# Performance work log

Hardware: AMD Instinct MI355X
Metric: run time of the kernel (lower is better)

Reference implementation:

```python
import jax, jax.numpy as jnp
import numpy as np
from functools import partial

RES = 512          # image resolution (source uses 1024; scaled for CPU baseline)
BLOB_COUNT = 2048  # number of Gaussian blobs (source uses 4096)
CHUNK = 64         # blobs processed per scan step to bound intermediates


def setup_inputs() -> dict:
    key = jax.random.key(0)
    k_pos, k_scale, k_rot, k_col = jax.random.split(key, 4)
    pos = jax.random.uniform(k_pos, (BLOB_COUNT, 2))                      # blob centers in [0,1]^2
    scale = 0.005 + 0.05 * jax.random.uniform(k_scale, (BLOB_COUNT, 2))   # per-axis std dev
    rot = 2.0 * jnp.pi * jax.random.uniform(k_rot, (BLOB_COUNT, 1))       # rotation angle
    color = jax.random.uniform(k_col, (BLOB_COUNT, 3))                    # rgb intensity
    blobs = jnp.concatenate([pos, scale, rot, color], axis=-1).astype(jnp.float32)  # [N, 8]
    return {"blobs": blobs}


def _splat(blobs):
    H = W = RES
    # pixel centers in normalized [0,1] coords
    ys = (jnp.arange(H, dtype=jnp.float32) + 0.5) / H
    xs = (jnp.arange(W, dtype=jnp.float32) + 0.5) / W
    py, px = jnp.meshgrid(ys, xs, indexing="ij")  # [H, W]

    def body(img, chunk):  # chunk: [CHUNK, 8]
        pos = chunk[:, 0:2]
        sx = chunk[:, 2][:, None, None]
        sy = chunk[:, 3][:, None, None]
        rot = chunk[:, 4]
        color = chunk[:, 5:8]
        c = jnp.cos(rot)[:, None, None]
        s = jnp.sin(rot)[:, None, None]
        dx = px[None] - pos[:, 0][:, None, None]   # [C, H, W]
        dy = py[None] - pos[:, 1][:, None, None]
        xr = c * dx + s * dy                        # rotate into blob frame
        yr = -s * dx + c * dy
        g = jnp.exp(-0.5 * ((xr / sx) ** 2 + (yr / sy) ** 2))  # [C, H, W]
        img = img + jnp.einsum("chw,ck->hwk", g, color)
        return img, None

    img0 = jnp.zeros((H, W, 3), dtype=blobs.dtype)
    chunks = blobs.reshape(BLOB_COUNT // CHUNK, CHUNK, 8)
    img, _ = jax.lax.scan(jax.checkpoint(body), img0, chunks)
    return img


@jax.jit
def reference(blobs):
    return _splat(blobs)
```

## Files before the change

kernel.cpp:

```cpp
#include <hip/hip_runtime.h>
#include <math.h>

#define RES     512
#define NBLOB   2048
#define TILE_W  32
#define TILE_H  32
#define ROWS_T  8
#define TX_N    (RES / TILE_W)
#define TY_N    (RES / TILE_H)
#define PRE_STRIDE 16
#define CHUNK_B 256
#define NCHUNK  (NBLOB / CHUNK_B)
#define CULL_R  4.4055f

__device__ __forceinline__ float fast_exp2(float x) {
#if __has_builtin(__builtin_amdgcn_exp2f)
    return __builtin_amdgcn_exp2f(x);
#else
    return exp2f(x);
#endif
}

__global__ __launch_bounds__(256) void pre_kernel(const float* __restrict__ blobs,
                                                  float* __restrict__ pre) {
    int i = blockIdx.x * blockDim.x + threadIdx.x;
    if (i >= NBLOB) return;
    const float* bp = blobs + i * 8;
    float posx = bp[0], posy = bp[1];
    float sx = bp[2], sy = bp[3];
    float rot = bp[4];
    float c = cosf(rot), s = sinf(rot);
    const float K = 0.84932184f;
    float isx = K / sx, isy = K / sy;
    float* o = pre + i * PRE_STRIDE;
    o[0] = posx;
    o[1] = posy;
    o[2] = c * isx;
    o[3] = s * isx;
    o[4] = -s * isy;
    o[5] = c * isy;
    o[6] = bp[5];
    o[7] = bp[6];
    o[8] = bp[7];
    o[9] = 0.f; o[10] = 0.f; o[11] = 0.f;

    float hx = CULL_R * sqrtf(c * c * sx * sx + s * s * sy * sy);
    float hy = CULL_R * sqrtf(s * s * sx * sx + c * c * sy * sy);
    int tx0 = max(0,        (int)floorf(((posx - hx) * RES - 0.5f) * (1.0f / TILE_W)));
    int tx1 = min(TX_N - 1, (int)floorf(((posx + hx) * RES - 0.5f) * (1.0f / TILE_W)));
    int ty0 = max(0,        (int)floorf(((posy - hy) * RES - 0.5f) * (1.0f / TILE_H)));
    int ty1 = min(TY_N - 1, (int)floorf(((posy + hy) * RES - 0.5f) * (1.0f / TILE_H)));
    int* ob = (int*)(o + 12);
    ob[0] = tx0; ob[1] = tx1; ob[2] = ty0; ob[3] = ty1;
}

__global__ __launch_bounds__(256) void splat_kernel(const float* __restrict__ pre,
                                                    float* __restrict__ out) {
    __shared__ int sh_cnt[NCHUNK];
    __shared__ float4 sh_p0[CHUNK_B];
    __shared__ float4 sh_p1[CHUNK_B];
    __shared__ float  sh_p2[CHUNK_B];

    const int tid = threadIdx.x;
    const int lane = tid & 63;
    const int tx = blockIdx.x;
    const int ty = blockIdx.y;

    if (tid < NCHUNK) sh_cnt[tid] = 0;

    const int x  = tx * TILE_W + (tid & 31);
    const int y0 = ty * TILE_H + (tid >> 5);
    const float fx  = (x + 0.5f) * (1.0f / RES);
    const float fy0 = (y0 + 0.5f) * (1.0f / RES);
    const float DY  = (float)ROWS_T * (1.0f / RES);

    float ar0 = 0.f, ag0 = 0.f, ab0 = 0.f;
    float ar1 = 0.f, ag1 = 0.f, ab1 = 0.f;
    float ar2 = 0.f, ag2 = 0.f, ab2 = 0.f;
    float ar3 = 0.f, ag3 = 0.f, ab3 = 0.f;

    __syncthreads();

    for (int c = 0; c < NCHUNK; ++c) {
        const int j = c * CHUNK_B + tid;
        const int4 ob = *(const int4*)(pre + j * PRE_STRIDE + 12);
        const bool hit = (tx >= ob.x) & (tx <= ob.y) & (ty >= ob.z) & (ty <= ob.w);
        const unsigned long long mask = __ballot(hit);
        const int total = __popcll(mask);
        int base = 0;
        if (lane == 0 && total > 0) base = atomicAdd(&sh_cnt[c], total);
        base = __builtin_amdgcn_readfirstlane(base);
        if (hit) {
            const int pos = base + __popcll(mask & ((1ull << lane) - 1ull));
            const float4* p4 = (const float4*)(pre + j * PRE_STRIDE);
            sh_p0[pos] = p4[0];
            sh_p1[pos] = p4[1];
            sh_p2[pos] = p4[2].x;
        }
        __syncthreads();

        const int n = sh_cnt[c];
        #pragma unroll 4
        for (int k = 0; k < n; ++k) {
            const float4 p0 = sh_p0[k];
            const float4 p1 = sh_p1[k];
            const float  cb = sh_p2[k];
            const float dx = fx - p0.x;
            const float dy = fy0 - p0.y;
            const float bD = p0.w * DY;
            const float eD = p1.y * DY;
            float u = p0.z * dx + p0.w * dy;
            float v = p1.x * dx + p1.y * dy;

            const float g0 = fast_exp2(-(u * u + v * v));
            u += bD; v += eD;
            const float g1 = fast_exp2(-(u * u + v * v));
            u += bD; v += eD;
            const float g2 = fast_exp2(-(u * u + v * v));
            u += bD; v += eD;
            const float g3 = fast_exp2(-(u * u + v * v));

            ar0 += g0 * p1.z;  ag0 += g0 * p1.w;  ab0 += g0 * cb;
            ar1 += g1 * p1.z;  ag1 += g1 * p1.w;  ab1 += g1 * cb;
            ar2 += g2 * p1.z;  ag2 += g2 * p1.w;  ab2 += g2 * cb;
            ar3 += g3 * p1.z;  ag3 += g3 * p1.w;  ab3 += g3 * cb;
        }
        __syncthreads();
    }

    const int b0 = (y0 * RES + x) * 3;
    out[b0 + 0] = ar0;  out[b0 + 1] = ag0;  out[b0 + 2] = ab0;
    const int b1 = ((y0 + ROWS_T) * RES + x) * 3;
    out[b1 + 0] = ar1;  out[b1 + 1] = ag1;  out[b1 + 2] = ab1;
    const int b2 = ((y0 + 2 * ROWS_T) * RES + x) * 3;
    out[b2 + 0] = ar2;  out[b2 + 1] = ag2;  out[b2 + 2] = ab2;
    const int b3 = ((y0 + 3 * ROWS_T) * RES + x) * 3;
    out[b3 + 0] = ar3;  out[b3 + 1] = ag3;  out[b3 + 2] = ab3;
}

extern "C" void kernel_launch(void* const* d_in, const int* in_sizes, int n_in,
                              void* d_out, int out_size, void* d_ws, size_t ws_size,
                              hipStream_t stream) {
    const float* blobs = (const float*)d_in[0];
    float* out = (float*)d_out;
    float* pre = (float*)d_ws;

    hipLaunchKernelGGL(pre_kernel, dim3(NBLOB / 256), dim3(256), 0, stream,
                       blobs, pre);
    hipLaunchKernelGGL(splat_kernel, dim3(TX_N, TY_N), dim3(256), 0, stream,
                       pre, out);
}
```

Measured before the change: 82.85 us.

## Fuse blob preprocessing into splat kernel and cull with elliptical tile test

Drops the separate preprocessing kernel. Each splat block now reads the raw blobs directly, computes sincos and the inverse-scale transform itself, and culls with a circle test in the blob's normalized frame around the tile center instead of the bounding-box tile ranges. This removes one kernel launch and the workspace round trip, and culls blobs more tightly. In exchange, every one of the 256 tiles recomputes the per-blob transcendental and division work, and the cull radius depends on a tile half-diagonal bound.

New measurement: 78.63 us. -5.1%, faster.

```diff
diff --git a/kernel.cpp b/kernel.cpp
--- a/kernel.cpp
+++ b/kernel.cpp
@@ -8,10 +8,11 @@
 #define ROWS_T  8
 #define TX_N    (RES / TILE_W)
 #define TY_N    (RES / TILE_H)
-#define PRE_STRIDE 16
 #define CHUNK_B 256
 #define NCHUNK  (NBLOB / CHUNK_B)
-#define CULL_R  4.4055f
+#define K_CONST   0.84932184f
+#define SQRT_CULL 3.7416574f
+#define HALFDIAG  0.0428132f
 
 __device__ __forceinline__ float fast_exp2(float x) {
 #if __has_builtin(__builtin_amdgcn_exp2f)
@@ -21,40 +22,7 @@
 #endif
 }
 
-__global__ __launch_bounds__(256) void pre_kernel(const float* __restrict__ blobs,
-                                                  float* __restrict__ pre) {
-    int i = blockIdx.x * blockDim.x + threadIdx.x;
-    if (i >= NBLOB) return;
-    const float* bp = blobs + i * 8;
-    float posx = bp[0], posy = bp[1];
-    float sx = bp[2], sy = bp[3];
-    float rot = bp[4];
-    float c = cosf(rot), s = sinf(rot);
-    const float K = 0.84932184f;
-    float isx = K / sx, isy = K / sy;
-    float* o = pre + i * PRE_STRIDE;
-    o[0] = posx;
-    o[1] = posy;
-    o[2] = c * isx;
-    o[3] = s * isx;
-    o[4] = -s * isy;
-    o[5] = c * isy;
-    o[6] = bp[5];
-    o[7] = bp[6];
-    o[8] = bp[7];
-    o[9] = 0.f; o[10] = 0.f; o[11] = 0.f;
-
-    float hx = CULL_R * sqrtf(c * c * sx * sx + s * s * sy * sy);
-    float hy = CULL_R * sqrtf(s * s * sx * sx + c * c * sy * sy);
-    int tx0 = max(0,        (int)floorf(((posx - hx) * RES - 0.5f) * (1.0f / TILE_W)));
-    int tx1 = min(TX_N - 1, (int)floorf(((posx + hx) * RES - 0.5f) * (1.0f / TILE_W)));
-    int ty0 = max(0,        (int)floorf(((posy - hy) * RES - 0.5f) * (1.0f / TILE_H)));
-    int ty1 = min(TY_N - 1, (int)floorf(((posy + hy) * RES - 0.5f) * (1.0f / TILE_H)));
-    int* ob = (int*)(o + 12);
-    ob[0] = tx0; ob[1] = tx1; ob[2] = ty0; ob[3] = ty1;
-}
-
-__global__ __launch_bounds__(256) void splat_kernel(const float* __restrict__ pre,
+__global__ __launch_bounds__(256) void splat_kernel(const float* __restrict__ blobs,
                                                     float* __restrict__ out) {
     __shared__ int sh_cnt[NCHUNK];
     __shared__ float4 sh_p0[CHUNK_B];
@@ -74,6 +42,9 @@
     const float fy0 = (y0 + 0.5f) * (1.0f / RES);
     const float DY  = (float)ROWS_T * (1.0f / RES);
 
+    const float cxT = (tx * TILE_W + 16.0f) * (1.0f / RES);
+    const float cyT = (ty * TILE_H + 16.0f) * (1.0f / RES);
+
     float ar0 = 0.f, ag0 = 0.f, ab0 = 0.f;
     float ar1 = 0.f, ag1 = 0.f, ab1 = 0.f;
     float ar2 = 0.f, ag2 = 0.f, ab2 = 0.f;
@@ -83,8 +54,25 @@
 
     for (int c = 0; c < NCHUNK; ++c) {
         const int j = c * CHUNK_B + tid;
-        const int4 ob = *(const int4*)(pre + j * PRE_STRIDE + 12);
-        const bool hit = (tx >= ob.x) & (tx <= ob.y) & (ty >= ob.z) & (ty <= ob.w);
+        const float4 b0 = *(const float4*)(blobs + j * 8);
+        const float4 b1 = *(const float4*)(blobs + j * 8 + 4);
+        const float sx = b0.z, sy = b0.w;
+        float sn, cn;
+        __sincosf(b1.x, &sn, &cn);
+        const float isx = K_CONST / sx;
+        const float isy = K_CONST / sy;
+        const float ma =  cn * isx;
+        const float mb =  sn * isx;
+        const float md = -sn * isy;
+        const float me =  cn * isy;
+        const float opn = K_CONST / fminf(sx, sy);
+        const float rt  = SQRT_CULL + opn * HALFDIAG;
+        const float dxc = cxT - b0.x;
+        const float dyc = cyT - b0.y;
+        const float uc = ma * dxc + mb * dyc;
+        const float vc = md * dxc + me * dyc;
+        const bool hit = fmaf(uc, uc, vc * vc) <= rt * rt;
+
         const unsigned long long mask = __ballot(hit);
         const int total = __popcll(mask);
         int base = 0;
@@ -92,10 +80,9 @@
         base = __builtin_amdgcn_readfirstlane(base);
         if (hit) {
             const int pos = base + __popcll(mask & ((1ull << lane) - 1ull));
-            const float4* p4 = (const float4*)(pre + j * PRE_STRIDE);
-            sh_p0[pos] = p4[0];
-            sh_p1[pos] = p4[1];
-            sh_p2[pos] = p4[2].x;
+            sh_p0[pos] = make_float4(b0.x, b0.y, ma, mb);
+            sh_p1[pos] = make_float4(md, me, b1.y, b1.z);
+            sh_p2[pos] = b1.w;
         }
         __syncthreads();
 
@@ -112,13 +99,13 @@
             float u = p0.z * dx + p0.w * dy;
             float v = p1.x * dx + p1.y * dy;
 
-            const float g0 = fast_exp2(-(u * u + v * v));
+            const float g0 = fast_exp2(-fmaf(u, u, v * v));
             u += bD; v += eD;
-            const float g1 = fast_exp2(-(u * u + v * v));
+            const float g1 = fast_exp2(-fmaf(u, u, v * v));
             u += bD; v += eD;
-            const float g2 = fast_exp2(-(u * u + v * v));
+            const float g2 = fast_exp2(-fmaf(u, u, v * v));
             u += bD; v += eD;
-            const float g3 = fast_exp2(-(u * u + v * v));
+            const float g3 = fast_exp2(-fmaf(u, u, v * v));
 
             ar0 += g0 * p1.z;  ag0 += g0 * p1.w;  ab0 += g0 * cb;
             ar1 += g1 * p1.z;  ag1 += g1 * p1.w;  ab1 += g1 * cb;
@@ -128,14 +115,14 @@
         __syncthreads();
     }
 
-    const int b0 = (y0 * RES + x) * 3;
-    out[b0 + 0] = ar0;  out[b0 + 1] = ag0;  out[b0 + 2] = ab0;
-    const int b1 = ((y0 + ROWS_T) * RES + x) * 3;
-    out[b1 + 0] = ar1;  out[b1 + 1] = ag1;  out[b1 + 2] = ab1;
-    const int b2 = ((y0 + 2 * ROWS_T) * RES + x) * 3;
-    out[b2 + 0] = ar2;  out[b2 + 1] = ag2;  out[b2 + 2] = ab2;
-    const int b3 = ((y0 + 3 * ROWS_T) * RES + x) * 3;
-    out[b3 + 0] = ar3;  out[b3 + 1] = ag3;  out[b3 + 2] = ab3;
+    const int b0i = (y0 * RES + x) * 3;
+    out[b0i + 0] = ar0;  out[b0i + 1] = ag0;  out[b0i + 2] = ab0;
+    const int b1i = ((y0 + ROWS_T) * RES + x) * 3;
+    out[b1i + 0] = ar1;  out[b1i + 1] = ag1;  out[b1i + 2] = ab1;
+    const int b2i = ((y0 + 2 * ROWS_T) * RES + x) * 3;
+    out[b2i + 0] = ar2;  out[b2i + 1] = ag2;  out[b2i + 2] = ab2;
+    const int b3i = ((y0 + 3 * ROWS_T) * RES + x) * 3;
+    out[b3i + 0] = ar3;  out[b3i + 1] = ag3;  out[b3i + 2] = ab3;
 }
 
 extern "C" void kernel_launch(void* const* d_in, const int* in_sizes, int n_in,
@@ -143,10 +130,8 @@
                               hipStream_t stream) {
     const float* blobs = (const float*)d_in[0];
     float* out = (float*)d_out;
-    float* pre = (float*)d_ws;
+    (void)d_ws; (void)ws_size;
 
-    hipLaunchKernelGGL(pre_kernel, dim3(NBLOB / 256), dim3(256), 0, stream,
-                       blobs, pre);
     hipLaunchKernelGGL(splat_kernel, dim3(TX_N, TY_N), dim3(256), 0, stream,
-                       pre, out);
+                       blobs, out);
 }
```
